# Optimization experiments

Measured on AMD Instinct MI355X. Metric: run time of the kernel, lower is better.

The kernel has to match this reference:

```python
import jax, jax.numpy as jnp
import numpy as np
import math

D_MODEL = 768
D_STATE = 16
D_CONV = 4
EXPAND = 2
D_INNER = EXPAND * D_MODEL        # 1536
DT_RANK = math.ceil(D_MODEL / 16) # 48
BATCH, SEQ = 2, 1024
EPS = 1e-6


def setup_inputs() -> dict:
    key = jax.random.key(0)
    ks = jax.random.split(key, 10)
    s = 0.02
    x = jax.random.normal(ks[0], (BATCH, SEQ, D_MODEL), dtype=jnp.float32)
    norm_w = jnp.ones((D_MODEL,), dtype=jnp.float32)
    in_proj_w = jax.random.normal(ks[1], (D_MODEL, 2 * D_INNER), dtype=jnp.float32) * s
    conv_w = jax.random.normal(ks[2], (D_INNER, D_CONV), dtype=jnp.float32) * 0.1
    conv_b = jnp.zeros((D_INNER,), dtype=jnp.float32)
    x_proj_w = jax.random.normal(ks[3], (D_INNER, DT_RANK + 2 * D_STATE), dtype=jnp.float32) * s
    dt_proj_w = jax.random.normal(ks[4], (DT_RANK, D_INNER), dtype=jnp.float32) * (DT_RANK ** -0.5)
    # dt bias init so softplus(dt_bias) ~ uniform in [1e-3, 1e-1] (mamba-style)
    dt = jnp.exp(jax.random.uniform(ks[5], (D_INNER,)) * (np.log(0.1) - np.log(1e-3)) + np.log(1e-3))
    dt_proj_b = dt + jnp.log(-jnp.expm1(-dt))  # inverse softplus
    A_log = jnp.log(jnp.broadcast_to(jnp.arange(1, D_STATE + 1, dtype=jnp.float32), (D_INNER, D_STATE)))
    D = jnp.ones((D_INNER,), dtype=jnp.float32)
    out_proj_w = jax.random.normal(ks[6], (D_INNER, D_MODEL), dtype=jnp.float32) * s
    return {"x": x, "norm_w": norm_w, "in_proj_w": in_proj_w, "conv_w": conv_w,
            "conv_b": conv_b, "x_proj_w": x_proj_w, "dt_proj_w": dt_proj_w,
            "dt_proj_b": dt_proj_b, "A_log": A_log, "D": D, "out_proj_w": out_proj_w}


def _rmsnorm(x, w):
    rms = jnp.sqrt(jnp.mean(x * x, axis=-1, keepdims=True) + EPS)
    return (x / rms) * w


def _causal_depthwise_conv(xi, conv_w, conv_b):
    # xi: (B, L, d_inner); depthwise causal conv over L with kernel D_CONV
    xp = jnp.pad(xi, ((0, 0), (D_CONV - 1, 0), (0, 0)))           # (B, L+K-1, C)
    kern = conv_w.T[:, None, :]                                     # (K, 1, C) -> HWIO with groups=C
    out = jax.lax.conv_general_dilated(
        xp, kern, window_strides=(1,), padding='VALID',
        dimension_numbers=('NWC', 'WIO', 'NWC'),
        feature_group_count=D_INNER)
    return out + conv_b


def _mamba_forward(x, norm_w, in_proj_w, conv_w, conv_b, x_proj_w,
                   dt_proj_w, dt_proj_b, A_log, D, out_proj_w):
    residual = x
    h = _rmsnorm(x, norm_w)
    xz = h @ in_proj_w                                   # (B, L, 2*d_inner)
    xi, z = jnp.split(xz, 2, axis=-1)
    xi = jax.nn.silu(_causal_depthwise_conv(xi, conv_w, conv_b))
    dbc = xi @ x_proj_w                                  # (B, L, dt_rank+2n)
    dt_low = dbc[..., :DT_RANK]
    Bm = dbc[..., DT_RANK:DT_RANK + D_STATE]             # (B, L, n)
    Cm = dbc[..., DT_RANK + D_STATE:]                    # (B, L, n)
    dt = jax.nn.softplus(dt_low @ dt_proj_w + dt_proj_b) # (B, L, d_inner)
    A = -jnp.exp(A_log)                                  # (d_inner, n)
    # discretize: a_t = exp(dt*A), b_t = dt * B_t * x_t   -> (B, L, d_inner, n)
    a = jnp.exp(dt[..., None] * A)
    b = (dt * xi)[..., None] * Bm[:, :, None, :]
    def combine(e1, e2):
        a1, b1 = e1
        a2, b2 = e2
        return a1 * a2, a2 * b1 + b2
    _, hstates = jax.lax.associative_scan(combine, (a, b), axis=1)
    y = jnp.einsum('bldn,bln->bld', hstates, Cm) + D * xi
    y = y * jax.nn.silu(z)
    return y @ out_proj_w + residual


def reference(x, norm_w, in_proj_w, conv_w, conv_b, x_proj_w,
              dt_proj_w, dt_proj_b, A_log, D, out_proj_w):
    return _mamba_forward(x, norm_w, in_proj_w, conv_w, conv_b, x_proj_w,
                          dt_proj_w, dt_proj_b, A_log, D, out_proj_w)
```

## Files before the change

kernel.cpp:

```cpp
#include <hip/hip_runtime.h>
#include <hip/hip_bf16.h>
#include <math.h>
#include <stdint.h>

#define D_MODEL 768
#define D_STATE 16
#define D_INNER 1536
#define DT_RANK 48
#define BATCH   2
#define SEQ     1024
#define NROWS   (BATCH*SEQ)
#define DBC_N   80
#define DBC_NP  128
#define NCHUNK  64
#define CHUNK   16
#define SCAN_G  (BATCH*NCHUNK*D_INNER)
#define SCAN_T  ((size_t)SCAN_G*D_STATE)

typedef short short8 __attribute__((ext_vector_type(8)));
typedef float floatx4 __attribute__((ext_vector_type(4)));

__device__ __forceinline__ float siluf(float x){ return x / (1.0f + __expf(-x)); }
__device__ __forceinline__ short f2b(float f){
    union { __hip_bfloat16 h; short s; } u; u.h = __float2bfloat16(f); return u.s;
}
__device__ __forceinline__ float b2f(short s){
    union { short s; __hip_bfloat16 h; } u; u.s = s; return __bfloat162float(u.h);
}
__device__ __forceinline__ void gload_lds16(const void* g, void* l){
    auto gp = reinterpret_cast<const __attribute__((address_space(1))) uint32_t*>(
        reinterpret_cast<uintptr_t>(g));
    auto lp = reinterpret_cast<__attribute__((address_space(3))) uint32_t*>(
        reinterpret_cast<uintptr_t>(l));
    __builtin_amdgcn_global_load_lds(gp, lp, 16, 0, 0);
}

__device__ __forceinline__ void transp32(const float* in, short* outT,
                                         int R, int C, int Cout,
                                         int bx, int by, int t,
                                         float (*tile)[33]){
    int c0 = bx*32, r0 = by*32;
    int tx = t & 31, ty = t >> 5;
    #pragma unroll
    for (int p = 0; p < 4; p++){
        int r = r0 + ty + p*8, c = c0 + tx;
        tile[ty+p*8][tx] = (r < R && c < C) ? in[(size_t)r*C + c] : 0.f;
    }
    __syncthreads();
    #pragma unroll
    for (int p = 0; p < 4; p++){
        int c = c0 + ty + p*8;
        int r = r0 + tx;
        if (c < Cout && r < R)
            outT[(size_t)c*R + r] = f2b(tile[tx][ty+p*8]);
    }
}

__global__ __launch_bounds__(256) void k_prep(const float* __restrict__ x,
                                              const float* __restrict__ nw,
                                              short* __restrict__ hb,
                                              const float* __restrict__ w1, short* __restrict__ Wb1,
                                              const float* __restrict__ w3, short* __restrict__ Wb3,
                                              const float* __restrict__ wx, short* __restrict__ Wbx,
                                              float* __restrict__ dbc){
    __shared__ float tile[32][33];
    int bid = blockIdx.x, t = threadIdx.x;
    if (bid < 2048){
        const float* xr = x + (size_t)bid * D_MODEL;
        float v[3]; float ss = 0.f;
        #pragma unroll
        for (int i = 0; i < 3; i++){ v[i] = xr[t + i*256]; ss += v[i]*v[i]; }
        #pragma unroll
        for (int o = 1; o < 64; o <<= 1) ss += __shfl_xor(ss, o, 64);
        int wave = t >> 6, lane = t & 63;
        if (lane == 0) tile[0][wave] = ss;
        __syncthreads();
        float tot = tile[0][0] + tile[0][1] + tile[0][2] + tile[0][3];
        float scale = rsqrtf(tot * (1.0f/768.0f) + 1e-6f);
        #pragma unroll
        for (int i = 0; i < 3; i++){
            int idx = t + i*256;
            hb[(size_t)bid*D_MODEL + idx] = f2b(v[i] * scale * nw[idx]);
        }
    } else if (bid < 4352){
        int id = bid - 2048;
        transp32(w1, Wb1, 768, 3072, 3072, id % 96, id / 96, t, tile);
    } else if (bid < 5504){
        int id = bid - 4352;
        transp32(w3, Wb3, 1536, 768, 768, id % 24, id / 24, t, tile);
    } else if (bid < 5696){
        int id = bid - 5504;
        transp32(wx, Wbx, 1536, DBC_N, DBC_NP, id % 4, id / 4, t, tile);
    } else {
        int id = bid - 5696;
        size_t base = (size_t)id*1024 + t*4;
        *(float4*)&dbc[base] = make_float4(0.f,0.f,0.f,0.f);
    }
}

template<int BM, int BN, int MODE, int KSPLIT>
__global__ __launch_bounds__(256) void k_mfma_bt(const short* __restrict__ A,
                                                 const short* __restrict__ Bt,
                                                 void* __restrict__ Cv,
                                                 const float* __restrict__ res,
                                                 int M, int N, int K, int Nld){
    constexpr int WM = BM/2, WN = BN/2;
    constexpr int FM = WM/16, FN = WN/16;
    constexpr int AU = BM*4;
    constexpr int BU = BN*4;
    __shared__ short As[BM*32];
    __shared__ short Bs[BN*32];
    int t = threadIdx.x;
    int wave = t >> 6, lane = t & 63;
    int lm = lane & 15, lq = lane >> 4;
    int row0 = blockIdx.y * BM, col0 = blockIdx.x * BN;
    int wr = (wave >> 1) * WM, wc = (wave & 1) * WN;
    int kper = K / KSPLIT;
    int kbeg = blockIdx.z * kper;
    floatx4 acc[FM][FN];
    #pragma unroll
    for (int mi = 0; mi < FM; mi++)
        #pragma unroll
        for (int ni = 0; ni < FN; ni++)
            acc[mi][ni] = (floatx4){0.f,0.f,0.f,0.f};

    for (int k0 = kbeg; k0 < kbeg + kper; k0 += 32){
        if constexpr (AU >= 256){
            #pragma unroll
            for (int r2 = 0; r2 < AU/256; r2++){
                int slot = r2*256 + t;
                int ar = slot >> 2, ak = (slot & 3)*8;
                gload_lds16(A + (size_t)(row0+ar)*K + k0 + ak, &As[slot*8]);
            }
        } else {
            if (t < AU){
                int ar = t >> 2, ak = (t & 3)*8;
                gload_lds16(A + (size_t)(row0+ar)*K + k0 + ak, &As[t*8]);
            }
        }
        if constexpr (BU >= 256){
            #pragma unroll
            for (int r2 = 0; r2 < BU/256; r2++){
                int slot = r2*256 + t;
                int br = slot >> 2, bk = (slot & 3)*8;
                gload_lds16(Bt + (size_t)(col0+br)*K + k0 + bk, &Bs[slot*8]);
            }
        } else {
            if (t < BU){
                int br = t >> 2, bk = (t & 3)*8;
                gload_lds16(Bt + (size_t)(col0+br)*K + k0 + bk, &Bs[t*8]);
            }
        }
        __syncthreads();
        short8 af[FM], bfr[FN];
        #pragma unroll
        for (int mi = 0; mi < FM; mi++)
            af[mi] = *(const short8*)&As[(wr + mi*16 + lm)*32 + lq*8];
        #pragma unroll
        for (int ni = 0; ni < FN; ni++)
            bfr[ni] = *(const short8*)&Bs[(wc + ni*16 + lm)*32 + lq*8];
        #pragma unroll
        for (int mi = 0; mi < FM; mi++)
            #pragma unroll
            for (int ni = 0; ni < FN; ni++)
                acc[mi][ni] = __builtin_amdgcn_mfma_f32_16x16x32_bf16(
                                  af[mi], bfr[ni], acc[mi][ni], 0, 0, 0);
        __syncthreads();
    }
    float* Cf = (float*)Cv;
    short* Cs = (short*)Cv;
    #pragma unroll
    for (int mi = 0; mi < FM; mi++)
        #pragma unroll
        for (int ni = 0; ni < FN; ni++)
            #pragma unroll
            for (int r = 0; r < 4; r++){
                int m = row0 + wr + mi*16 + lq*4 + r;
                int n = col0 + wc + ni*16 + lm;
                float v = acc[mi][ni][r];
                if constexpr (MODE == 0){
                    Cf[(size_t)m*Nld + n] = v;
                } else if constexpr (MODE == 1){
                    Cf[(size_t)m*Nld + n] = v + res[(size_t)m*Nld + n];
                } else if constexpr (MODE == 2){
                    Cs[(size_t)m*Nld + n] = f2b(v);
                } else {
                    if (n < Nld) atomicAdd(&Cf[(size_t)m*Nld + n], v);
                }
            }
}

__global__ __launch_bounds__(256) void k_conv(const short* __restrict__ xzb,
                                              const float* __restrict__ cw,
                                              const float* __restrict__ cb,
                                              short* __restrict__ xcb){
    int idx = blockIdx.x * 256 + threadIdx.x;
    int d = idx % D_INNER;
    int r = idx / D_INNER;
    int l = r % SEQ;
    float acc = cb[d];
    #pragma unroll
    for (int k = 0; k < 4; k++){
        int ls = l - 3 + k;
        if (ls >= 0)
            acc += b2f(xzb[(size_t)(r - 3 + k)*3072 + d]) * cw[d*4 + k];
    }
    xcb[idx] = f2b(siluf(acc));
}


__global__ __launch_bounds__(256) void k_scanA(const short* __restrict__ xcb,
                                               const float* __restrict__ dbc,
                                               const float* __restrict__ wdt,
                                               const float* __restrict__ bdt,
                                               const float* __restrict__ A_log,
                                               float* __restrict__ Aprod,
                                               float* __restrict__ Hloc,
                                               short* __restrict__ dtb){
    int t = blockIdx.x * 256 + threadIdx.x;
    int d = t % D_INNER;
    int bc = t / D_INNER;
    int chunk = bc % NCHUNK, b = bc / NCHUNK;
    int r0 = b*SEQ + chunk*CHUNK;

    float dt16[CHUNK];
    {
        float wr[DT_RANK];
        #pragma unroll
        for (int k = 0; k < DT_RANK; k++) wr[k] = wdt[k*D_INNER + d];
        float bj = bdt[d];
        for (int l = 0; l < CHUNK; l++){
            const float* dl = &dbc[(size_t)(r0+l)*DBC_N];
            float acc = bj;
            #pragma unroll
            for (int k = 0; k < DT_RANK; k++) acc += dl[k] * wr[k];
            float sp = (acc > 20.f) ? acc : __logf(1.f + __expf(acc));
            dt16[l] = sp;
            dtb[(size_t)(r0+l)*D_INNER + d] = f2b(sp);
        }
    }

    float A[16], h[16], aP[16];
    const float4* al = (const float4*)&A_log[d*D_STATE];
    #pragma unroll
    for (int i = 0; i < 4; i++){
        float4 v = al[i];
        A[4*i+0] = -__expf(v.x); A[4*i+1] = -__expf(v.y);
        A[4*i+2] = -__expf(v.z); A[4*i+3] = -__expf(v.w);
    }
    #pragma unroll
    for (int n = 0; n < 16; n++){ h[n] = 0.f; aP[n] = 1.f; }
    for (int l = 0; l < CHUNK; l++){
        int r = r0 + l;
        float dtv = dt16[l];
        float xcv = b2f(xcb[(size_t)r*D_INNER + d]);
        const float4* bp = (const float4*)&dbc[(size_t)r*DBC_N + DT_RANK];
        float Bm[16];
        #pragma unroll
        for (int i = 0; i < 4; i++){
            float4 v = bp[i];
            Bm[4*i+0]=v.x; Bm[4*i+1]=v.y; Bm[4*i+2]=v.z; Bm[4*i+3]=v.w;
        }
        float comm = dtv * xcv;
        #pragma unroll
        for (int n = 0; n < 16; n++){
            float a = __expf(dtv * A[n]);
            h[n] = a*h[n] + comm*Bm[n];
            aP[n] *= a;
        }
    }
    float4* ap = (float4*)&Aprod[(size_t)t*16];
    float4* hp = (float4*)&Hloc[(size_t)t*16];
    #pragma unroll
    for (int i = 0; i < 4; i++){
        ap[i] = make_float4(aP[4*i], aP[4*i+1], aP[4*i+2], aP[4*i+3]);
        hp[i] = make_float4(h[4*i], h[4*i+1], h[4*i+2], h[4*i+3]);
    }
}

__global__ __launch_bounds__(256) void k_scanB(const float* Aprod,
                                               const float* Hloc,
                                               float* carry){
    int t = blockIdx.x * 256 + threadIdx.x;
    int dn = t % (D_INNER*16);
    int b  = t / (D_INNER*16);
    float c = 0.f;
    #pragma unroll 4
    for (int ch = 0; ch < NCHUNK; ch++){
        size_t idx = ((size_t)((b*NCHUNK + ch)*D_INNER))*16 + dn;
        float a  = Aprod[idx];
        float hl = Hloc[idx];
        carry[idx] = c;
        c = a*c + hl;
    }
}

__global__ __launch_bounds__(256) void k_scanC(const short* __restrict__ dtb,
                                               const short* __restrict__ xcb,
                                               const float* __restrict__ dbc,
                                               const short* __restrict__ xzb,
                                               const float* __restrict__ A_log,
                                               const float* __restrict__ Dp,
                                               const float* __restrict__ carry,
                                               short* __restrict__ yb){
    int t = blockIdx.x * 256 + threadIdx.x;
    int d = t % D_INNER;
    int bc = t / D_INNER;
    int chunk = bc % NCHUNK, b = bc / NCHUNK;
    float A[16], h[16];
    const float4* al = (const float4*)&A_log[d*D_STATE];
    #pragma unroll
    for (int i = 0; i < 4; i++){
        float4 v = al[i];
        A[4*i+0] = -__expf(v.x); A[4*i+1] = -__expf(v.y);
        A[4*i+2] = -__expf(v.z); A[4*i+3] = -__expf(v.w);
    }
    const float4* cp = (const float4*)&carry[(size_t)t*16];
    #pragma unroll
    for (int i = 0; i < 4; i++){
        float4 v = cp[i];
        h[4*i+0]=v.x; h[4*i+1]=v.y; h[4*i+2]=v.z; h[4*i+3]=v.w;
    }
    float Dv = Dp[d];
    int r0 = b*SEQ + chunk*CHUNK;
    for (int l = 0; l < CHUNK; l++){
        int r = r0 + l;
        float dtv = b2f(dtb[(size_t)r*D_INNER + d]);
        float xcv = b2f(xcb[(size_t)r*D_INNER + d]);
        const float4* bp = (const float4*)&dbc[(size_t)r*DBC_N + DT_RANK];
        float Bm[16], Cm[16];
        #pragma unroll
        for (int i = 0; i < 4; i++){
            float4 v = bp[i];
            Bm[4*i+0]=v.x; Bm[4*i+1]=v.y; Bm[4*i+2]=v.z; Bm[4*i+3]=v.w;
            float4 w = bp[4+i];
            Cm[4*i+0]=w.x; Cm[4*i+1]=w.y; Cm[4*i+2]=w.z; Cm[4*i+3]=w.w;
        }
        float comm = dtv * xcv;
        float yv = 0.f;
        #pragma unroll
        for (int n = 0; n < 16; n++){
            float a = __expf(dtv * A[n]);
            h[n] = a*h[n] + comm*Bm[n];
            yv += h[n]*Cm[n];
        }
        float z = b2f(xzb[(size_t)r*(2*D_INNER) + D_INNER + d]);
        yb[(size_t)r*D_INNER + d] = f2b((yv + Dv*xcv) * siluf(z));
    }
}

extern "C" void kernel_launch(void* const* d_in, const int* in_sizes, int n_in,
                              void* d_out, int out_size, void* d_ws, size_t ws_size,
                              hipStream_t stream) {
    const float* x         = (const float*)d_in[0];
    const float* norm_w    = (const float*)d_in[1];
    const float* in_proj_w = (const float*)d_in[2];
    const float* conv_w    = (const float*)d_in[3];
    const float* conv_b    = (const float*)d_in[4];
    const float* x_proj_w  = (const float*)d_in[5];
    const float* dt_proj_w = (const float*)d_in[6];
    const float* dt_proj_b = (const float*)d_in[7];
    const float* A_log     = (const float*)d_in[8];
    const float* Dp        = (const float*)d_in[9];
    const float* out_proj_w= (const float*)d_in[10];
    float* out = (float*)d_out;

    char* p = (char*)d_ws;
    short* hb  = (short*)p; p += (size_t)NROWS*D_MODEL*2;
    short* xzb = (short*)p; p += (size_t)NROWS*3072*2;
    short* xcb = (short*)p; p += (size_t)NROWS*D_INNER*2;
    float* dbc = (float*)p; p += (size_t)NROWS*DBC_N*4;
    short* dtb = (short*)p; p += (size_t)NROWS*D_INNER*2;
    short* yb  = (short*)p; p += (size_t)NROWS*D_INNER*2;
    float* Ap  = (float*)p; p += SCAN_T*4;
    float* Hl  = (float*)p; p += SCAN_T*4;
    short* Wb1 = (short*)p; p += (size_t)3072*768*2;
    short* Wb3 = (short*)p; p += (size_t)768*1536*2;
    short* Wbx = (short*)p; p += (size_t)DBC_NP*1536*2;
    float* cr  = Ap;

    k_prep<<<5856, 256, 0, stream>>>(x, norm_w, hb, in_proj_w, Wb1,
                                     out_proj_w, Wb3, x_proj_w, Wbx, dbc);

    k_mfma_bt<128,64,2,1><<<dim3(3072/64, NROWS/128), 256, 0, stream>>>(
        hb, Wb1, xzb, nullptr, NROWS, 3072, D_MODEL, 3072);

    k_conv<<<(NROWS*D_INNER)/256, 256, 0, stream>>>(xzb, conv_w, conv_b, xcb);

    k_mfma_bt<64,64,3,8><<<dim3(DBC_NP/64, NROWS/64, 8), 256, 0, stream>>>(
        xcb, Wbx, dbc, nullptr, NROWS, DBC_NP, D_INNER, DBC_N);

    k_scanA<<<SCAN_G/256, 256, 0, stream>>>(xcb, dbc, dt_proj_w, dt_proj_b,
                                            A_log, Ap, Hl, dtb);
    k_scanB<<<(BATCH*D_INNER*D_STATE)/256, 256, 0, stream>>>(Ap, Hl, cr);
    k_scanC<<<SCAN_G/256, 256, 0, stream>>>(dtb, xcb, dbc, xzb, A_log, Dp,
                                            cr, yb);

    k_mfma_bt<64,64,1,1><<<dim3(768/64, NROWS/64), 256, 0, stream>>>(
        yb, Wb3, out, x, NROWS, 768, D_INNER, 768);
}
```

Measured before the change: 238.1 us.

## Fuse conv into x_proj GEMM, store scan carries in bf16, split-K out_proj

The causal depthwise conv plus SiLU is computed inside the split-K x_proj GEMM's A-tile load, which removes a separate kernel launch and the re-read of xcb. Because grid.x is 2, each conv element is computed twice, and both column blocks write the same values to xcb. The chunk-scan intermediates (Aprod, Hloc, carry) are now stored as bf16, halving their memory traffic at the cost of reduced precision in the state carry. The out_proj GEMM becomes 2-way split-K with atomic accumulation into an output that k_prep pre-initialises with the residual x.

```diff
diff --git a/kernel.cpp b/kernel.cpp
--- a/kernel.cpp
+++ b/kernel.cpp
@@ -62,7 +62,8 @@
                                               const float* __restrict__ w1, short* __restrict__ Wb1,
                                               const float* __restrict__ w3, short* __restrict__ Wb3,
                                               const float* __restrict__ wx, short* __restrict__ Wbx,
-                                              float* __restrict__ dbc){
+                                              float* __restrict__ dbc,
+                                              float* __restrict__ out){
     __shared__ float tile[32][33];
     int bid = blockIdx.x, t = threadIdx.x;
     if (bid < 2048){
@@ -91,10 +92,17 @@
     } else if (bid < 5696){
         int id = bid - 5504;
         transp32(wx, Wbx, 1536, DBC_N, DBC_NP, id % 4, id / 4, t, tile);
-    } else {
+    } else if (bid < 5856){
         int id = bid - 5696;
         size_t base = (size_t)id*1024 + t*4;
         *(float4*)&dbc[base] = make_float4(0.f,0.f,0.f,0.f);
+    } else {
+        int id = bid - 5856;
+        #pragma unroll
+        for (int p = 0; p < 4; p++){
+            size_t off = (size_t)id*4096 + p*1024 + t*4;
+            *(float4*)&out[off] = *(const float4*)&x[off];
+        }
     }
 }
 
@@ -178,9 +186,7 @@
                 int m = row0 + wr + mi*16 + lq*4 + r;
                 int n = col0 + wc + ni*16 + lm;
                 float v = acc[mi][ni][r];
-                if constexpr (MODE == 0){
-                    Cf[(size_t)m*Nld + n] = v;
-                } else if constexpr (MODE == 1){
+                if constexpr (MODE == 1){
                     Cf[(size_t)m*Nld + n] = v + res[(size_t)m*Nld + n];
                 } else if constexpr (MODE == 2){
                     Cs[(size_t)m*Nld + n] = f2b(v);
@@ -190,22 +196,77 @@
             }
 }
 
-__global__ __launch_bounds__(256) void k_conv(const short* __restrict__ xzb,
-                                              const float* __restrict__ cw,
-                                              const float* __restrict__ cb,
-                                              short* __restrict__ xcb){
-    int idx = blockIdx.x * 256 + threadIdx.x;
-    int d = idx % D_INNER;
-    int r = idx / D_INNER;
-    int l = r % SEQ;
-    float acc = cb[d];
-    #pragma unroll
-    for (int k = 0; k < 4; k++){
-        int ls = l - 3 + k;
-        if (ls >= 0)
-            acc += b2f(xzb[(size_t)(r - 3 + k)*3072 + d]) * cw[d*4 + k];
-    }
-    xcb[idx] = f2b(siluf(acc));
+__global__ __launch_bounds__(256) void k_xproj_conv(const short* __restrict__ xzb,
+                                                    const float* __restrict__ cw,
+                                                    const float* __restrict__ cb,
+                                                    const short* __restrict__ Bt,
+                                                    float* __restrict__ dbc,
+                                                    short* __restrict__ xcb){
+    __shared__ short As[64*32];
+    __shared__ short Bs[64*32];
+    int t = threadIdx.x;
+    int wave = t >> 6, lane = t & 63;
+    int lm = lane & 15, lq = lane >> 4;
+    int row0 = blockIdx.y * 64, col0 = blockIdx.x * 64;
+    int wr = (wave >> 1) * 32, wc = (wave & 1) * 32;
+    int kbeg = blockIdx.z * (D_INNER/8);
+    floatx4 acc[2][2];
+    #pragma unroll
+    for (int mi = 0; mi < 2; mi++)
+        #pragma unroll
+        for (int ni = 0; ni < 2; ni++)
+            acc[mi][ni] = (floatx4){0.f,0.f,0.f,0.f};
+
+    for (int k0 = kbeg; k0 < kbeg + D_INNER/8; k0 += 32){
+        {
+            int br = t >> 2, bk = (t & 3)*8;
+            gload_lds16(Bt + (size_t)(col0+br)*D_INNER + k0 + bk, &Bs[t*8]);
+        }
+        #pragma unroll
+        for (int e8 = 0; e8 < 8; e8++){
+            int e = e8*256 + t;
+            int row = e >> 5, dcol = e & 31;
+            int d = k0 + dcol;
+            int r = row0 + row;
+            int l = r & (SEQ-1);
+            float acc2 = cb[d];
+            #pragma unroll
+            for (int k = 0; k < 4; k++){
+                int lt = l - 3 + k;
+                if (lt >= 0)
+                    acc2 += b2f(xzb[(size_t)(r-3+k)*3072 + d]) * cw[d*4 + k];
+            }
+            short sv = f2b(siluf(acc2));
+            As[e] = sv;
+            xcb[(size_t)r*D_INNER + d] = sv;
+        }
+        __syncthreads();
+        short8 af[2], bfr[2];
+        #pragma unroll
+        for (int mi = 0; mi < 2; mi++)
+            af[mi] = *(const short8*)&As[(wr + mi*16 + lm)*32 + lq*8];
+        #pragma unroll
+        for (int ni = 0; ni < 2; ni++)
+            bfr[ni] = *(const short8*)&Bs[(wc + ni*16 + lm)*32 + lq*8];
+        #pragma unroll
+        for (int mi = 0; mi < 2; mi++)
+            #pragma unroll
+            for (int ni = 0; ni < 2; ni++)
+                acc[mi][ni] = __builtin_amdgcn_mfma_f32_16x16x32_bf16(
+                                  af[mi], bfr[ni], acc[mi][ni], 0, 0, 0);
+        __syncthreads();
+    }
+    #pragma unroll
+    for (int mi = 0; mi < 2; mi++)
+        #pragma unroll
+        for (int ni = 0; ni < 2; ni++)
+            #pragma unroll
+            for (int r = 0; r < 4; r++){
+                int m = row0 + wr + mi*16 + lq*4 + r;
+                int n = col0 + wc + ni*16 + lm;
+                if (n < DBC_N)
+                    atomicAdd(&dbc[(size_t)m*DBC_N + n], acc[mi][ni][r]);
+            }
 }
 
 
@@ -214,8 +275,8 @@
                                                const float* __restrict__ wdt,
                                                const float* __restrict__ bdt,
                                                const float* __restrict__ A_log,
-                                               float* __restrict__ Aprod,
-                                               float* __restrict__ Hloc,
+                                               short* __restrict__ Apb,
+                                               short* __restrict__ Hlb,
                                                short* __restrict__ dtb){
     int t = blockIdx.x * 256 + threadIdx.x;
     int d = t % D_INNER;
@@ -269,18 +330,20 @@
             aP[n] *= a;
         }
     }
-    float4* ap = (float4*)&Aprod[(size_t)t*16];
-    float4* hp = (float4*)&Hloc[(size_t)t*16];
-    #pragma unroll
-    for (int i = 0; i < 4; i++){
-        ap[i] = make_float4(aP[4*i], aP[4*i+1], aP[4*i+2], aP[4*i+3]);
-        hp[i] = make_float4(h[4*i], h[4*i+1], h[4*i+2], h[4*i+3]);
-    }
-}
-
-__global__ __launch_bounds__(256) void k_scanB(const float* Aprod,
-                                               const float* Hloc,
-                                               float* carry){
+    short8 s0, s1;
+    #pragma unroll
+    for (int i = 0; i < 8; i++){ s0[i] = f2b(aP[i]);  s1[i] = f2b(aP[8+i]); }
+    *(short8*)&Apb[(size_t)t*16]     = s0;
+    *(short8*)&Apb[(size_t)t*16 + 8] = s1;
+    #pragma unroll
+    for (int i = 0; i < 8; i++){ s0[i] = f2b(h[i]);   s1[i] = f2b(h[8+i]); }
+    *(short8*)&Hlb[(size_t)t*16]     = s0;
+    *(short8*)&Hlb[(size_t)t*16 + 8] = s1;
+}
+
+__global__ __launch_bounds__(256) void k_scanB(const short* Apb,
+                                               const short* Hlb,
+                                               short* carry){
     int t = blockIdx.x * 256 + threadIdx.x;
     int dn = t % (D_INNER*16);
     int b  = t / (D_INNER*16);
@@ -288,9 +351,9 @@
     #pragma unroll 4
     for (int ch = 0; ch < NCHUNK; ch++){
         size_t idx = ((size_t)((b*NCHUNK + ch)*D_INNER))*16 + dn;
-        float a  = Aprod[idx];
-        float hl = Hloc[idx];
-        carry[idx] = c;
+        float a  = b2f(Apb[idx]);
+        float hl = b2f(Hlb[idx]);
+        carry[idx] = f2b(c);
         c = a*c + hl;
     }
 }
@@ -301,7 +364,7 @@
                                                const short* __restrict__ xzb,
                                                const float* __restrict__ A_log,
                                                const float* __restrict__ Dp,
-                                               const float* __restrict__ carry,
+                                               const short* __restrict__ carry,
                                                short* __restrict__ yb){
     int t = blockIdx.x * 256 + threadIdx.x;
     int d = t % D_INNER;
@@ -315,11 +378,11 @@
         A[4*i+0] = -__expf(v.x); A[4*i+1] = -__expf(v.y);
         A[4*i+2] = -__expf(v.z); A[4*i+3] = -__expf(v.w);
     }
-    const float4* cp = (const float4*)&carry[(size_t)t*16];
-    #pragma unroll
-    for (int i = 0; i < 4; i++){
-        float4 v = cp[i];
-        h[4*i+0]=v.x; h[4*i+1]=v.y; h[4*i+2]=v.z; h[4*i+3]=v.w;
+    {
+        short8 c0 = *(const short8*)&carry[(size_t)t*16];
+        short8 c1 = *(const short8*)&carry[(size_t)t*16 + 8];
+        #pragma unroll
+        for (int i = 0; i < 8; i++){ h[i] = b2f(c0[i]); h[8+i] = b2f(c1[i]); }
     }
     float Dv = Dp[d];
     int r0 = b*SEQ + chunk*CHUNK;
@@ -372,30 +435,28 @@
     float* dbc = (float*)p; p += (size_t)NROWS*DBC_N*4;
     short* dtb = (short*)p; p += (size_t)NROWS*D_INNER*2;
     short* yb  = (short*)p; p += (size_t)NROWS*D_INNER*2;
-    float* Ap  = (float*)p; p += SCAN_T*4;
-    float* Hl  = (float*)p; p += SCAN_T*4;
+    short* Apb = (short*)p; p += SCAN_T*2;
+    short* Hlb = (short*)p; p += SCAN_T*2;
     short* Wb1 = (short*)p; p += (size_t)3072*768*2;
     short* Wb3 = (short*)p; p += (size_t)768*1536*2;
     short* Wbx = (short*)p; p += (size_t)DBC_NP*1536*2;
-    float* cr  = Ap;
-
-    k_prep<<<5856, 256, 0, stream>>>(x, norm_w, hb, in_proj_w, Wb1,
-                                     out_proj_w, Wb3, x_proj_w, Wbx, dbc);
+    short* cr  = Apb;
+
+    k_prep<<<6240, 256, 0, stream>>>(x, norm_w, hb, in_proj_w, Wb1,
+                                     out_proj_w, Wb3, x_proj_w, Wbx, dbc, out);
 
     k_mfma_bt<128,64,2,1><<<dim3(3072/64, NROWS/128), 256, 0, stream>>>(
         hb, Wb1, xzb, nullptr, NROWS, 3072, D_MODEL, 3072);
 
-    k_conv<<<(NROWS*D_INNER)/256, 256, 0, stream>>>(xzb, conv_w, conv_b, xcb);
-
-    k_mfma_bt<64,64,3,8><<<dim3(DBC_NP/64, NROWS/64, 8), 256, 0, stream>>>(
-        xcb, Wbx, dbc, nullptr, NROWS, DBC_NP, D_INNER, DBC_N);
+    k_xproj_conv<<<dim3(DBC_NP/64, NROWS/64, 8), 256, 0, stream>>>(
+        xzb, conv_w, conv_b, Wbx, dbc, xcb);
 
     k_scanA<<<SCAN_G/256, 256, 0, stream>>>(xcb, dbc, dt_proj_w, dt_proj_b,
-                                            A_log, Ap, Hl, dtb);
-    k_scanB<<<(BATCH*D_INNER*D_STATE)/256, 256, 0, stream>>>(Ap, Hl, cr);
+                                            A_log, Apb, Hlb, dtb);
+    k_scanB<<<(BATCH*D_INNER*D_STATE)/256, 256, 0, stream>>>(Apb, Hlb, cr);
     k_scanC<<<SCAN_G/256, 256, 0, stream>>>(dtb, xcb, dbc, xzb, A_log, Dp,
                                             cr, yb);
 
-    k_mfma_bt<64,64,1,1><<<dim3(768/64, NROWS/64), 256, 0, stream>>>(
-        yb, Wb3, out, x, NROWS, 768, D_INNER, 768);
-}
+    k_mfma_bt<64,64,3,2><<<dim3(768/64, NROWS/64, 2), 256, 0, stream>>>(
+        yb, Wb3, out, nullptr, NROWS, 768, D_INNER, 768);
+}
```

Result: slower. 251.0 us (+5.4%).

## Store scan chunk state in bf16 and split-K out_proj with atomic residual

Applied to the files above, without the earlier changes.

The per-chunk decay products, local states and carries of the chunked scan are now stored as bf16 instead of fp32, halving the traffic of the scan intermediates between the three scan kernels. The residual is copied into the output buffer during the prep kernel, and the output projection switches to a 2-way split-K with atomicAdd accumulation onto it. This raises parallelism for the small out_proj GEMM. It risks precision loss in the carried scan state and adds atomic contention plus nondeterministic summation order.

```diff
diff --git a/kernel.cpp b/kernel.cpp
--- a/kernel.cpp
+++ b/kernel.cpp
@@ -62,7 +62,8 @@
                                               const float* __restrict__ w1, short* __restrict__ Wb1,
                                               const float* __restrict__ w3, short* __restrict__ Wb3,
                                               const float* __restrict__ wx, short* __restrict__ Wbx,
-                                              float* __restrict__ dbc){
+                                              float* __restrict__ dbc,
+                                              float* __restrict__ out){
     __shared__ float tile[32][33];
     int bid = blockIdx.x, t = threadIdx.x;
     if (bid < 2048){
@@ -91,10 +92,17 @@
     } else if (bid < 5696){
         int id = bid - 5504;
         transp32(wx, Wbx, 1536, DBC_N, DBC_NP, id % 4, id / 4, t, tile);
-    } else {
+    } else if (bid < 5856){
         int id = bid - 5696;
         size_t base = (size_t)id*1024 + t*4;
         *(float4*)&dbc[base] = make_float4(0.f,0.f,0.f,0.f);
+    } else {
+        int id = bid - 5856;
+        #pragma unroll
+        for (int p = 0; p < 4; p++){
+            size_t off = (size_t)id*4096 + p*1024 + t*4;
+            *(float4*)&out[off] = *(const float4*)&x[off];
+        }
     }
 }
 
@@ -102,7 +110,6 @@
 __global__ __launch_bounds__(256) void k_mfma_bt(const short* __restrict__ A,
                                                  const short* __restrict__ Bt,
                                                  void* __restrict__ Cv,
-                                                 const float* __restrict__ res,
                                                  int M, int N, int K, int Nld){
     constexpr int WM = BM/2, WN = BN/2;
     constexpr int FM = WM/16, FN = WN/16;
@@ -178,11 +185,7 @@
                 int m = row0 + wr + mi*16 + lq*4 + r;
                 int n = col0 + wc + ni*16 + lm;
                 float v = acc[mi][ni][r];
-                if constexpr (MODE == 0){
-                    Cf[(size_t)m*Nld + n] = v;
-                } else if constexpr (MODE == 1){
-                    Cf[(size_t)m*Nld + n] = v + res[(size_t)m*Nld + n];
-                } else if constexpr (MODE == 2){
+                if constexpr (MODE == 2){
                     Cs[(size_t)m*Nld + n] = f2b(v);
                 } else {
                     if (n < Nld) atomicAdd(&Cf[(size_t)m*Nld + n], v);
@@ -214,8 +217,8 @@
                                                const float* __restrict__ wdt,
                                                const float* __restrict__ bdt,
                                                const float* __restrict__ A_log,
-                                               float* __restrict__ Aprod,
-                                               float* __restrict__ Hloc,
+                                               short* __restrict__ Apb,
+                                               short* __restrict__ Hlb,
                                                short* __restrict__ dtb){
     int t = blockIdx.x * 256 + threadIdx.x;
     int d = t % D_INNER;
@@ -269,18 +272,20 @@
             aP[n] *= a;
         }
     }
-    float4* ap = (float4*)&Aprod[(size_t)t*16];
-    float4* hp = (float4*)&Hloc[(size_t)t*16];
-    #pragma unroll
-    for (int i = 0; i < 4; i++){
-        ap[i] = make_float4(aP[4*i], aP[4*i+1], aP[4*i+2], aP[4*i+3]);
-        hp[i] = make_float4(h[4*i], h[4*i+1], h[4*i+2], h[4*i+3]);
-    }
-}
-
-__global__ __launch_bounds__(256) void k_scanB(const float* Aprod,
-                                               const float* Hloc,
-                                               float* carry){
+    short8 s0, s1;
+    #pragma unroll
+    for (int i = 0; i < 8; i++){ s0[i] = f2b(aP[i]);  s1[i] = f2b(aP[8+i]); }
+    *(short8*)&Apb[(size_t)t*16]     = s0;
+    *(short8*)&Apb[(size_t)t*16 + 8] = s1;
+    #pragma unroll
+    for (int i = 0; i < 8; i++){ s0[i] = f2b(h[i]);   s1[i] = f2b(h[8+i]); }
+    *(short8*)&Hlb[(size_t)t*16]     = s0;
+    *(short8*)&Hlb[(size_t)t*16 + 8] = s1;
+}
+
+__global__ __launch_bounds__(256) void k_scanB(const short* Apb,
+                                               const short* Hlb,
+                                               short* carry){
     int t = blockIdx.x * 256 + threadIdx.x;
     int dn = t % (D_INNER*16);
     int b  = t / (D_INNER*16);
@@ -288,9 +293,9 @@
     #pragma unroll 4
     for (int ch = 0; ch < NCHUNK; ch++){
         size_t idx = ((size_t)((b*NCHUNK + ch)*D_INNER))*16 + dn;
-        float a  = Aprod[idx];
-        float hl = Hloc[idx];
-        carry[idx] = c;
+        float a  = b2f(Apb[idx]);
+        float hl = b2f(Hlb[idx]);
+        carry[idx] = f2b(c);
         c = a*c + hl;
     }
 }
@@ -301,7 +306,7 @@
                                                const short* __restrict__ xzb,
                                                const float* __restrict__ A_log,
                                                const float* __restrict__ Dp,
-                                               const float* __restrict__ carry,
+                                               const short* __restrict__ carry,
                                                short* __restrict__ yb){
     int t = blockIdx.x * 256 + threadIdx.x;
     int d = t % D_INNER;
@@ -315,11 +320,11 @@
         A[4*i+0] = -__expf(v.x); A[4*i+1] = -__expf(v.y);
         A[4*i+2] = -__expf(v.z); A[4*i+3] = -__expf(v.w);
     }
-    const float4* cp = (const float4*)&carry[(size_t)t*16];
-    #pragma unroll
-    for (int i = 0; i < 4; i++){
-        float4 v = cp[i];
-        h[4*i+0]=v.x; h[4*i+1]=v.y; h[4*i+2]=v.z; h[4*i+3]=v.w;
+    {
+        short8 c0 = *(const short8*)&carry[(size_t)t*16];
+        short8 c1 = *(const short8*)&carry[(size_t)t*16 + 8];
+        #pragma unroll
+        for (int i = 0; i < 8; i++){ h[i] = b2f(c0[i]); h[8+i] = b2f(c1[i]); }
     }
     float Dv = Dp[d];
     int r0 = b*SEQ + chunk*CHUNK;
@@ -372,30 +377,30 @@
     float* dbc = (float*)p; p += (size_t)NROWS*DBC_N*4;
     short* dtb = (short*)p; p += (size_t)NROWS*D_INNER*2;
     short* yb  = (short*)p; p += (size_t)NROWS*D_INNER*2;
-    float* Ap  = (float*)p; p += SCAN_T*4;
-    float* Hl  = (float*)p; p += SCAN_T*4;
+    short* Apb = (short*)p; p += SCAN_T*2;
+    short* Hlb = (short*)p; p += SCAN_T*2;
     short* Wb1 = (short*)p; p += (size_t)3072*768*2;
     short* Wb3 = (short*)p; p += (size_t)768*1536*2;
     short* Wbx = (short*)p; p += (size_t)DBC_NP*1536*2;
-    float* cr  = Ap;
-
-    k_prep<<<5856, 256, 0, stream>>>(x, norm_w, hb, in_proj_w, Wb1,
-                                     out_proj_w, Wb3, x_proj_w, Wbx, dbc);
+    short* cr  = Apb;
+
+    k_prep<<<6240, 256, 0, stream>>>(x, norm_w, hb, in_proj_w, Wb1,
+                                     out_proj_w, Wb3, x_proj_w, Wbx, dbc, out);
 
     k_mfma_bt<128,64,2,1><<<dim3(3072/64, NROWS/128), 256, 0, stream>>>(
-        hb, Wb1, xzb, nullptr, NROWS, 3072, D_MODEL, 3072);
+        hb, Wb1, xzb, NROWS, 3072, D_MODEL, 3072);
 
     k_conv<<<(NROWS*D_INNER)/256, 256, 0, stream>>>(xzb, conv_w, conv_b, xcb);
 
     k_mfma_bt<64,64,3,8><<<dim3(DBC_NP/64, NROWS/64, 8), 256, 0, stream>>>(
-        xcb, Wbx, dbc, nullptr, NROWS, DBC_NP, D_INNER, DBC_N);
+        xcb, Wbx, dbc, NROWS, DBC_NP, D_INNER, DBC_N);
 
     k_scanA<<<SCAN_G/256, 256, 0, stream>>>(xcb, dbc, dt_proj_w, dt_proj_b,
-                                            A_log, Ap, Hl, dtb);
-    k_scanB<<<(BATCH*D_INNER*D_STATE)/256, 256, 0, stream>>>(Ap, Hl, cr);
+                                            A_log, Apb, Hlb, dtb);
+    k_scanB<<<(BATCH*D_INNER*D_STATE)/256, 256, 0, stream>>>(Apb, Hlb, cr);
     k_scanC<<<SCAN_G/256, 256, 0, stream>>>(dtb, xcb, dbc, xzb, A_log, Dp,
                                             cr, yb);
 
-    k_mfma_bt<64,64,1,1><<<dim3(768/64, NROWS/64), 256, 0, stream>>>(
-        yb, Wb3, out, x, NROWS, 768, D_INNER, 768);
-}
+    k_mfma_bt<64,64,3,2><<<dim3(768/64, NROWS/64, 2), 256, 0, stream>>>(
+        yb, Wb3, out, NROWS, 768, D_INNER, 768);
+}
```

Measured after the change: 232.6 us. 2.3% less time.
